# Performance work log

Measured on AMD Instinct MI355X. Metric: run time of the kernel, lower is better.

The kernel has to match this reference:

```python
import jax, jax.numpy as jnp
import numpy as np

DIM, N_HEADS, N_KV, HEAD_DIM = 4096, 32, 8, 128
REPEATS = N_HEADS // N_KV
SCALE = HEAD_DIM ** -0.5


def apply_rope(x, offset=0):
    # x: [b, h, l, hd]; rotation convention matches the torch source:
    # out_even = xe*cos + xo*sin, out_odd = -xe*sin + xo*cos, interleaved back.
    hd = x.shape[-1]
    l = x.shape[2]
    freqs = 1.0 / 10000.0 ** (jnp.arange(0, hd, 2, dtype=jnp.float32) / hd)  # [hd/2]
    t = jnp.arange(l, dtype=jnp.float32) + offset
    ang = t[:, None] * freqs[None, :]                     # [l, hd/2]
    sin, cos = jnp.sin(ang), jnp.cos(ang)
    xe, xo = x[..., 0::2], x[..., 1::2]                   # [b,h,l,hd/2]
    out = jnp.stack([xe * cos + xo * sin, -xe * sin + xo * cos], axis=-1)
    return out.reshape(x.shape)


def setup_inputs() -> dict:
    key = jax.random.key(0)
    ks = jax.random.split(key, 5)
    b, l = 1, 2048
    x = jax.random.normal(ks[0], (b, l, DIM), dtype=jnp.float32)
    # additive causal mask: 0 on/below diagonal, -1e9 above
    neg = jnp.full((l, l), -1e9, dtype=jnp.float32)
    mask = jnp.triu(neg, k=1)
    wq = jax.random.normal(ks[1], (N_HEADS * HEAD_DIM, DIM), dtype=jnp.float32) * 0.02
    wk = jax.random.normal(ks[2], (N_KV * HEAD_DIM, DIM), dtype=jnp.float32) * 0.02
    wv = jax.random.normal(ks[3], (N_KV * HEAD_DIM, DIM), dtype=jnp.float32) * 0.02
    wo = jax.random.normal(ks[4], (DIM, N_HEADS * HEAD_DIM), dtype=jnp.float32) * 0.02
    return {"x": x, "mask": mask, "wq": wq, "wk": wk, "wv": wv, "wo": wo}


def reference(x, mask, wq, wk, wv, wo):
    b, l, d = x.shape
    q = (x @ wq.T).reshape(b, l, N_HEADS, HEAD_DIM).transpose(0, 2, 1, 3)  # [b,H,l,hd]
    k = (x @ wk.T).reshape(b, l, N_KV, HEAD_DIM).transpose(0, 2, 1, 3)     # [b,Hk,l,hd]
    v = (x @ wv.T).reshape(b, l, N_KV, HEAD_DIM).transpose(0, 2, 1, 3)
    # GQA repeat (head = kv_head*repeats + r, same as torch cat+view)
    k = jnp.repeat(k, REPEATS, axis=1)
    v = jnp.repeat(v, REPEATS, axis=1)
    q = apply_rope(q)
    k = apply_rope(k)
    atn = jnp.einsum('bhqd,bhkd->bhqk', q * SCALE, k) + mask
    atn = jax.nn.softmax(atn.astype(jnp.float32), axis=-1).astype(q.dtype)
    out = jnp.einsum('bhqk,bhkd->bhqd', atn, v)
    out = out.transpose(0, 2, 1, 3).reshape(b, l, -1)
    return (out @ wo.T, k, v)
```

## Files before the change

kernel.cpp:

```cpp
#include <hip/hip_runtime.h>
#include <stdint.h>

#define L_SEQ  2048
#define NHEAD  32
#define NKV    8
#define HD     128
#define DIM    4096
#define KVDIM  1024
#define QKVS   6144
#define SCALE  0.08838834764831845f
#define LOG2E  1.4426950408889634f
#define SM_OFF 12.0f

typedef __attribute__((ext_vector_type(8))) short bf16x8;
typedef __attribute__((ext_vector_type(4))) float f32x4;

__device__ __forceinline__ unsigned short f2bf(float f) {
    unsigned u = __float_as_uint(f);
    u = (u + 0x7FFFu + ((u >> 16) & 1u)) >> 16;
    return (unsigned short)u;
}
__device__ __forceinline__ float bf2f(unsigned short h) {
    return __uint_as_float(((unsigned)h) << 16);
}
__device__ __forceinline__ void gload_lds16(const void* g, void* l) {
    __builtin_amdgcn_global_load_lds(
        (const __attribute__((address_space(1))) unsigned int*)g,
        (__attribute__((address_space(3))) unsigned int*)l, 16, 0, 0);
}

__global__ void cvt_f32_bf16(const float* __restrict__ in, unsigned short* __restrict__ out, int n4) {
    int i = blockIdx.x * blockDim.x + threadIdx.x;
    int stride = gridDim.x * blockDim.x;
    for (; i < n4; i += stride) {
        float4 v = ((const float4*)in)[i];
        ushort4 o;
        o.x = f2bf(v.x); o.y = f2bf(v.y); o.z = f2bf(v.z); o.w = f2bf(v.w);
        ((ushort4*)out)[i] = o;
    }
}

__global__ void addf32(float* __restrict__ out, const float* __restrict__ p, int n4) {
    int i = blockIdx.x * blockDim.x + threadIdx.x;
    int stride = gridDim.x * blockDim.x;
    for (; i < n4; i += stride) {
        float4 a = ((const float4*)out)[i];
        float4 b = ((const float4*)p)[i];
        a.x += b.x; a.y += b.y; a.z += b.z; a.w += b.w;
        ((float4*)out)[i] = a;
    }
}

__global__ void rope_table(float2* __restrict__ rt) {
    int i = blockIdx.x * blockDim.x + threadIdx.x;
    if (i >= L_SEQ * 64) return;
    int l = i >> 6, f = i & 63;
    float freq = powf(10000.0f, -(float)f / 64.0f);
    float ang  = (float)l * freq;
    rt[i] = make_float2(cosf(ang), sinf(ang));
}

__global__ void rope_apply(unsigned short* __restrict__ X, const float2* __restrict__ rt,
                           int log2H, int strideShorts, float mul) {
    int i = blockIdx.x * blockDim.x + threadIdx.x;
    int f  = i & 63;
    int hh = (i >> 6) & ((1 << log2H) - 1);
    int l  = i >> (6 + log2H);
    if (l >= L_SEQ) return;
    float2 cs = rt[(l << 6) + f];
    size_t base = (size_t)l * strideShorts + (hh << 7);
    float xe = bf2f(X[base + 2 * f]);
    float xo = bf2f(X[base + 2 * f + 1]);
    X[base + 2 * f]     = f2bf((xe * cs.x + xo * cs.y) * mul);
    X[base + 2 * f + 1] = f2bf((-xe * cs.y + xo * cs.x) * mul);
}

__global__ void kv_out(const unsigned short* __restrict__ KVp,
                       float* __restrict__ KO, float* __restrict__ VO) {
    int i = blockIdx.x * blockDim.x + threadIdx.x;
    if (i >= L_SEQ * KVDIM) return;
    int d  = i & 127;
    int h8 = (i >> 7) & 7;
    int l  = i >> 10;
    float kv = bf2f(KVp[(size_t)l * QKVS + h8 * HD + d]);
    float vv = bf2f(KVp[(size_t)l * QKVS + KVDIM + h8 * HD + d]);
#pragma unroll
    for (int r = 0; r < 4; ++r) {
        int h = h8 * 4 + r;
        KO[((size_t)h * L_SEQ + l) * HD + d] = kv;
        VO[((size_t)h * L_SEQ + l) * HD + d] = vv;
    }
}

__global__ void vtrans(const unsigned short* __restrict__ KVp, unsigned short* __restrict__ VT) {
    __shared__ unsigned short t[32][33];
    int lt = blockIdx.x * 32;
    int h8 = blockIdx.y >> 2;
    int dt = (blockIdx.y & 3) * 32;
    int tx = threadIdx.x & 31, ty = threadIdx.x >> 5;
#pragma unroll
    for (int yy = ty; yy < 32; yy += 8)
        t[yy][tx] = KVp[(size_t)(lt + yy) * QKVS + KVDIM + h8 * HD + dt + tx];
    __syncthreads();
#pragma unroll
    for (int yy = ty; yy < 32; yy += 8)
        VT[(size_t)(h8 * HD + dt + yy) * L_SEQ + lt + tx] = t[tx][yy];
}

template <typename OT>
__global__ __launch_bounds__(512, 2) void gemm_8ph(const unsigned short* __restrict__ A,
                                                   const unsigned short* __restrict__ B,
                                                   OT* __restrict__ C0, OT* __restrict__ C1,
                                                   int N, int K, int klen) {
    __shared__ __align__(16) char L[131072];
    const int tid = threadIdx.x;
    const int w = tid >> 6, lane = tid & 63;
    const int gx = gridDim.x;
    const int nwg = gx * gridDim.y;
    const int orig = blockIdx.y * gx + blockIdx.x;
    const int swz = (orig & 7) * (nwg >> 3) + (orig >> 3);
    const int m0 = (swz / gx) * 256, n0 = (swz % gx) * 256;
    const int kbase = blockIdx.z * klen;
    OT* __restrict__ C = blockIdx.z ? C1 : C0;
    const int wr = (w >> 2) & 1;
    const int wc = w & 3;
    const int lr = lane & 15, lg = lane >> 4;
    const int NKT = klen >> 6;

    auto stageA = [&](int slot, int half, int kt) {
#pragma unroll
        for (int c = 0; c < 2; ++c) {
            int rl = half * 128 + w * 16 + c * 8;
            int r  = rl + (lane >> 3);
            int cg = (lane & 7) ^ (r & 7);
            gload_lds16(A + (size_t)(m0 + r) * K + kbase + kt * 64 + cg * 8,
                        L + slot * 32768 + rl * 128);
        }
    };
    auto stageB = [&](int slot, int half, int kt) {
#pragma unroll
        for (int c = 0; c < 2; ++c) {
            int rl = half * 128 + w * 16 + c * 8;
            int r  = rl + (lane >> 3);
            int cg = (lane & 7) ^ (r & 7);
            gload_lds16(B + (size_t)(n0 + r) * K + kbase + kt * 64 + cg * 8,
                        L + 65536 + slot * 32768 + rl * 128);
        }
    };

    const f32x4 fz = {0.f, 0.f, 0.f, 0.f};
    f32x4 acc[8][4];
#pragma unroll
    for (int m = 0; m < 8; ++m)
#pragma unroll
        for (int n = 0; n < 4; ++n) acc[m][n] = fz;

    stageA(0, 0, 0); stageA(0, 1, 0); stageB(0, 0, 0); stageB(0, 1, 0);
    if (NKT > 1) { stageB(1, 0, 1); stageB(1, 1, 1); }
    asm volatile("s_waitcnt vmcnt(4)" ::: "memory");
    __builtin_amdgcn_s_barrier();

    const int swb = (lr & 7) << 4;
    bf16x8 bfrag[4][2];
    for (int kt = 0; kt < NKT; ++kt) {
        const int s = kt & 1;
        const char* Abase = L + s * 32768;
        const char* Bbase = L + 65536 + s * 32768;
#pragma unroll
        for (int q = 0; q < 4; ++q) {
            bf16x8 af[2][2];
#pragma unroll
            for (int mm = 0; mm < 2; ++mm)
#pragma unroll
                for (int kk = 0; kk < 2; ++kk) {
                    int r = wr * 128 + (q * 2 + mm) * 16 + lr;
                    int b = (kk * 64 + lg * 16) ^ swb;
                    af[mm][kk] = *(const bf16x8*)(Abase + r * 128 + b);
                }
            if (q == 0) {
#pragma unroll
                for (int n = 0; n < 4; ++n)
#pragma unroll
                    for (int kk = 0; kk < 2; ++kk) {
                        int r = wc * 64 + n * 16 + lr;
                        int b = (kk * 64 + lg * 16) ^ swb;
                        bfrag[n][kk] = *(const bf16x8*)(Bbase + r * 128 + b);
                    }
            }
            if (q == 0 && kt + 1 < NKT) stageA(s ^ 1, 0, kt + 1);
            if (q == 1 && kt + 1 < NKT) stageA(s ^ 1, 1, kt + 1);
            if (q == 2 && kt + 2 < NKT) stageB(s, 0, kt + 2);
            if (q == 3) {
                if (kt + 2 < NKT) stageB(s, 1, kt + 2);
                asm volatile("s_waitcnt vmcnt(4)" ::: "memory");
            }
            __builtin_amdgcn_s_barrier();
            asm volatile("s_waitcnt lgkmcnt(0)" ::: "memory");
            __builtin_amdgcn_sched_barrier(0);
            __builtin_amdgcn_s_setprio(1);
#pragma unroll
            for (int mm = 0; mm < 2; ++mm)
#pragma unroll
                for (int n = 0; n < 4; ++n)
#pragma unroll
                    for (int kk = 0; kk < 2; ++kk)
                        acc[q * 2 + mm][n] = __builtin_amdgcn_mfma_f32_16x16x32_bf16(
                            af[mm][kk], bfrag[n][kk], acc[q * 2 + mm][n], 0, 0, 0);
            __builtin_amdgcn_s_setprio(0);
            __builtin_amdgcn_s_barrier();
        }
    }
#pragma unroll
    for (int m = 0; m < 8; ++m) {
        int mrow = m0 + wr * 128 + m * 16 + lg * 4;
#pragma unroll
        for (int n = 0; n < 4; ++n) {
            int ncol = n0 + wc * 64 + n * 16 + lr;
#pragma unroll
            for (int r = 0; r < 4; ++r) {
                float v = acc[m][n][r];
                if constexpr (sizeof(OT) == 2) C[(size_t)(mrow + r) * N + ncol] = f2bf(v);
                else                           C[(size_t)(mrow + r) * N + ncol] = v;
            }
        }
    }
}

__global__ __launch_bounds__(128) void attn_fwd(const unsigned short* __restrict__ Q,
                                                const unsigned short* __restrict__ KVp,
                                                const unsigned short* __restrict__ VT,
                                                unsigned short* __restrict__ AO) {
    __shared__ __align__(16) unsigned short Ks[64 * 128];
    __shared__ __align__(16) unsigned short Vs[128 * 64];
    __shared__ __align__(16) unsigned short P[2][2][16][64];
    const int tid = threadIdx.x, w = tid >> 6, lane = tid & 63;
    const int idx = blockIdx.x;
    const int h8  = idx & 7;
    const int h   = (h8 << 2) + ((idx >> 3) & 3);
    const int u   = idx >> 5;
    const int t   = u & 7, quart = u >> 3;
    const int qb  = (quart == 0) ? 31 - t : (quart == 1) ? 16 + t
                  : (quart == 2) ? 15 - t : t;
    const int lr = lane & 15, lg = lane >> 4;
    const int r0 = qb * 64 + w * 32;

    bf16x8 qf[2][4];
#pragma unroll
    for (int f = 0; f < 2; ++f) {
        const unsigned short* qrow = Q + (size_t)(r0 + f * 16 + lr) * QKVS + h * HD + lg * 8;
#pragma unroll
        for (int kd = 0; kd < 4; ++kd) qf[f][kd] = *(const bf16x8*)(qrow + kd * 32);
    }

    bf16x8 ones;
#pragma unroll
    for (int z = 0; z < 8; ++z) ones[z] = (short)0x3F80;

    const f32x4 fz = {0.f, 0.f, 0.f, 0.f};
    f32x4 o[2][9];
#pragma unroll
    for (int f = 0; f < 2; ++f)
#pragma unroll
        for (int nd = 0; nd < 9; ++nd) o[f][nd] = fz;

    const int nkv = qb + 1;
    for (int kv = 0; kv < nkv; ++kv) {
        const int kv0 = kv * 64;
#pragma unroll
        for (int c = 0; c < 8; ++c) {
            int krow = w * 32 + c * 4 + (lane >> 4);
            int kcg  = (lane & 15) ^ (krow & 7);
            gload_lds16(KVp + (size_t)(kv0 + krow) * QKVS + h8 * HD + kcg * 8,
                        Ks + (w * 32 + c * 4) * 128);
            int vrow = w * 64 + c * 8 + (lane >> 3);
            int vcg  = (lane & 7) ^ (vrow & 7);
            gload_lds16(VT + (size_t)(h8 * HD + vrow) * L_SEQ + kv0 + vcg * 8,
                        Vs + (w * 64 + c * 8) * 64);
        }
        __syncthreads();
        f32x4 s[2][4];
#pragma unroll
        for (int f = 0; f < 2; ++f)
#pragma unroll
            for (int ni = 0; ni < 4; ++ni) s[f][ni] = fz;
        __builtin_amdgcn_s_setprio(1);
#pragma unroll
        for (int ni = 0; ni < 4; ++ni) {
            bf16x8 kf[4];
#pragma unroll
            for (int kd = 0; kd < 4; ++kd)
                kf[kd] = *(const bf16x8*)(Ks + (ni * 16 + lr) * 128 +
                                          (((kd * 4 + lg) ^ (lr & 7)) * 8));
#pragma unroll
            for (int f = 0; f < 2; ++f)
#pragma unroll
                for (int kd = 0; kd < 4; ++kd)
                    s[f][ni] = __builtin_amdgcn_mfma_f32_16x16x32_bf16(qf[f][kd], kf[kd], s[f][ni], 0, 0, 0);
        }
        __builtin_amdgcn_s_setprio(0);
#pragma unroll
        for (int f = 0; f < 2; ++f) {
            const int rbase = r0 + f * 16;
            const bool need_mask = (kv0 + 63) > rbase;
#pragma unroll
            for (int ni = 0; ni < 4; ++ni)
#pragma unroll
                for (int rr = 0; rr < 4; ++rr) {
                    float p = __builtin_amdgcn_exp2f(s[f][ni][rr] - SM_OFF);
                    if (need_mask) {
                        int col = kv0 + ni * 16 + lr;
                        int row = rbase + lg * 4 + rr;
                        p = (col > row) ? 0.f : p;
                    }
                    s[f][ni][rr] = p;
                }
            char* Pb = (char*)&P[w][f][0][0];
#pragma unroll
            for (int ni = 0; ni < 4; ni += 2)
#pragma unroll
                for (int rr = 0; rr < 4; ++rr) {
                    unsigned pk;
                    asm("v_cvt_pk_bf16_f32 %0, %1, %2" : "=v"(pk) : "v"(s[f][ni][rr]), "v"(s[f][ni + 1][rr]));
                    const int row = lg * 4 + rr;
                    const int sw = (row & 7) << 4;
                    *(unsigned short*)(Pb + ((row * 128 + (ni * 16 + lr) * 2) ^ sw)) = (unsigned short)pk;
                    *(unsigned short*)(Pb + ((row * 128 + ((ni + 1) * 16 + lr) * 2) ^ sw)) =
                        (unsigned short)(pk >> 16);
                }
        }
        bf16x8 pa[2][2];
        const int swr = (lr & 7) << 4;
#pragma unroll
        for (int f = 0; f < 2; ++f) {
            const char* Pb = (const char*)&P[w][f][0][0];
#pragma unroll
            for (int ks = 0; ks < 2; ++ks)
                pa[f][ks] = *(const bf16x8*)(Pb + ((lr * 128 + ks * 64 + lg * 16) ^ swr));
        }
        __builtin_amdgcn_s_setprio(1);
#pragma unroll
        for (int nd = 0; nd < 8; ++nd) {
            bf16x8 vf[2];
#pragma unroll
            for (int ks = 0; ks < 2; ++ks)
                vf[ks] = *(const bf16x8*)(Vs + (nd * 16 + lr) * 64 +
                                          (((ks * 4 + lg) ^ (lr & 7)) * 8));
#pragma unroll
            for (int f = 0; f < 2; ++f)
#pragma unroll
                for (int ks = 0; ks < 2; ++ks)
                    o[f][nd] = __builtin_amdgcn_mfma_f32_16x16x32_bf16(pa[f][ks], vf[ks], o[f][nd], 0, 0, 0);
        }
#pragma unroll
        for (int f = 0; f < 2; ++f)
#pragma unroll
            for (int ks = 0; ks < 2; ++ks)
                o[f][8] = __builtin_amdgcn_mfma_f32_16x16x32_bf16(pa[f][ks], ones, o[f][8], 0, 0, 0);
        __builtin_amdgcn_s_setprio(0);
        __syncthreads();
    }
#pragma unroll
    for (int f = 0; f < 2; ++f) {
        float inv[4];
#pragma unroll
        for (int rr = 0; rr < 4; ++rr) inv[rr] = 1.0f / o[f][8][rr];
#pragma unroll
        for (int nd = 0; nd < 8; ++nd)
#pragma unroll
            for (int rr = 0; rr < 4; ++rr) {
                int row = r0 + f * 16 + lg * 4 + rr;
                AO[(size_t)row * DIM + h * HD + nd * 16 + lr] = f2bf(o[f][nd][rr] * inv[rr]);
            }
    }
}

extern "C" void kernel_launch(void* const* d_in, const int* in_sizes, int n_in,
                              void* d_out, int out_size, void* d_ws, size_t ws_size,
                              hipStream_t stream) {
    (void)in_sizes; (void)n_in; (void)out_size; (void)ws_size;
    const float* x  = (const float*)d_in[0];
    const float* wq = (const float*)d_in[2];
    const float* wk = (const float*)d_in[3];
    const float* wv = (const float*)d_in[4];
    const float* wo = (const float*)d_in[5];

    float* out = (float*)d_out;
    float* KO  = out + (size_t)L_SEQ * DIM;
    float* VO  = KO + (size_t)NHEAD * L_SEQ * HD;

    char* ws = (char*)d_ws;
    const size_t MB = 1024 * 1024;
    unsigned short* xb   = (unsigned short*)(ws);
    unsigned short* wqb  = (unsigned short*)(ws + 16 * MB);
    unsigned short* wkvb = (unsigned short*)(ws + 48 * MB);
    unsigned short* qkvp = (unsigned short*)(ws + 64 * MB);
    unsigned short* vtb  = (unsigned short*)(ws + 88 * MB);
    float2*         rt   = (float2*)(ws + 92 * MB);
    unsigned short* aob  = xb;
    unsigned short* wob  = wqb;
    unsigned short* kvp  = qkvp + KVDIM * 4;
    float*          pko  = (float*)(ws + 48 * MB);

    cvt_f32_bf16<<<2048, 256, 0, stream>>>(x,  xb,  L_SEQ * DIM / 4);
    cvt_f32_bf16<<<2048, 256, 0, stream>>>(wq, wqb, DIM * DIM / 4);
    cvt_f32_bf16<<<2048, 256, 0, stream>>>(wk, wkvb, KVDIM * DIM / 4);
    cvt_f32_bf16<<<2048, 256, 0, stream>>>(wv, wkvb + (size_t)KVDIM * DIM, KVDIM * DIM / 4);
    rope_table<<<(L_SEQ * 64) / 256, 256, 0, stream>>>(rt);

    gemm_8ph<unsigned short><<<dim3(QKVS / 256, L_SEQ / 256, 1), 512, 0, stream>>>(
        xb, wqb, qkvp, qkvp, QKVS, DIM, DIM);
    cvt_f32_bf16<<<2048, 256, 0, stream>>>(wo, wob, DIM * DIM / 4);

    rope_apply<<<(L_SEQ * NHEAD * 64) / 256, 256, 0, stream>>>(qkvp, rt, 5, QKVS, SCALE * LOG2E);
    rope_apply<<<(L_SEQ * NKV * 64) / 256, 256, 0, stream>>>(kvp, rt, 3, QKVS, 1.0f);

    kv_out<<<(L_SEQ * KVDIM) / 256, 256, 0, stream>>>(kvp, KO, VO);
    vtrans<<<dim3(L_SEQ / 32, 32), 256, 0, stream>>>(kvp, vtb);

    attn_fwd<<<1024, 128, 0, stream>>>(qkvp, kvp, vtb, aob);

    gemm_8ph<float><<<dim3(DIM / 256, L_SEQ / 256, 2), 512, 0, stream>>>(
        aob, wob, out, pko, DIM, DIM, DIM / 2);
    addf32<<<2048, 256, 0, stream>>>(out, pko, L_SEQ * DIM / 4);
}
```

Before: 345.9 us.

## Double-buffer A fragments in registers to overlap LDS reads with MFMA

Restructures the GEMM main loop so the A-fragment LDS reads for the next quarter, and for the next k-tile's first quarter, are issued before the MFMA block of the current quarter. It also unrolls k-tiles in pairs so the LDS slot index is a compile-time constant. The global-to-LDS staging points and vmcnt waits are reordered to fit the new schedule. The aim is to hide LDS read latency behind matrix math. It costs extra VGPRs for the second fragment buffer, and the removed explicit lgkmcnt waits and sched_barriers leave ordering to the compiler, which risks correctness or spills under launch_bounds(512,2). The paired loop also assumes NKT is even.

```diff
diff --git a/kernel.cpp b/kernel.cpp
--- a/kernel.cpp
+++ b/kernel.cpp
@@ -126,6 +126,7 @@
     const int wc = w & 3;
     const int lr = lane & 15, lg = lane >> 4;
     const int NKT = klen >> 6;
+    const int swb = (lr & 7) << 4;
 
     auto stageA = [&](int slot, int half, int kt) {
 #pragma unroll
@@ -155,58 +156,81 @@
 #pragma unroll
         for (int n = 0; n < 4; ++n) acc[m][n] = fz;
 
+    bf16x8 af0[2][2], af1[2][2];
+    bf16x8 bfr[4][2];
+
+    auto readA = [&](bf16x8 (&dst)[2][2], const char* base, int q) {
+#pragma unroll
+        for (int mm = 0; mm < 2; ++mm)
+#pragma unroll
+            for (int kk = 0; kk < 2; ++kk) {
+                int r = wr * 128 + (q * 2 + mm) * 16 + lr;
+                int b = (kk * 64 + lg * 16) ^ swb;
+                dst[mm][kk] = *(const bf16x8*)(base + r * 128 + b);
+            }
+    };
+    auto readB = [&](const char* base) {
+#pragma unroll
+        for (int n = 0; n < 4; ++n)
+#pragma unroll
+            for (int kk = 0; kk < 2; ++kk) {
+                int r = wc * 64 + n * 16 + lr;
+                int b = (kk * 64 + lg * 16) ^ swb;
+                bfr[n][kk] = *(const bf16x8*)(base + r * 128 + b);
+            }
+    };
+    auto mfma16 = [&](int q, bf16x8 (&a)[2][2]) {
+        __builtin_amdgcn_s_setprio(1);
+#pragma unroll
+        for (int mm = 0; mm < 2; ++mm)
+#pragma unroll
+            for (int n = 0; n < 4; ++n)
+#pragma unroll
+                for (int kk = 0; kk < 2; ++kk)
+                    acc[q * 2 + mm][n] = __builtin_amdgcn_mfma_f32_16x16x32_bf16(
+                        a[mm][kk], bfr[n][kk], acc[q * 2 + mm][n], 0, 0, 0);
+        __builtin_amdgcn_s_setprio(0);
+    };
+
     stageA(0, 0, 0); stageA(0, 1, 0); stageB(0, 0, 0); stageB(0, 1, 0);
     if (NKT > 1) { stageB(1, 0, 1); stageB(1, 1, 1); }
     asm volatile("s_waitcnt vmcnt(4)" ::: "memory");
     __builtin_amdgcn_s_barrier();
-
-    const int swb = (lr & 7) << 4;
-    bf16x8 bfrag[4][2];
-    for (int kt = 0; kt < NKT; ++kt) {
-        const int s = kt & 1;
-        const char* Abase = L + s * 32768;
-        const char* Bbase = L + 65536 + s * 32768;
-#pragma unroll
-        for (int q = 0; q < 4; ++q) {
-            bf16x8 af[2][2];
-#pragma unroll
-            for (int mm = 0; mm < 2; ++mm)
-#pragma unroll
-                for (int kk = 0; kk < 2; ++kk) {
-                    int r = wr * 128 + (q * 2 + mm) * 16 + lr;
-                    int b = (kk * 64 + lg * 16) ^ swb;
-                    af[mm][kk] = *(const bf16x8*)(Abase + r * 128 + b);
-                }
-            if (q == 0) {
-#pragma unroll
-                for (int n = 0; n < 4; ++n)
-#pragma unroll
-                    for (int kk = 0; kk < 2; ++kk) {
-                        int r = wc * 64 + n * 16 + lr;
-                        int b = (kk * 64 + lg * 16) ^ swb;
-                        bfrag[n][kk] = *(const bf16x8*)(Bbase + r * 128 + b);
-                    }
+    readA(af0, L + 0, 0);
+
+    for (int kt0 = 0; kt0 < NKT; kt0 += 2) {
+#pragma unroll
+        for (int kp = 0; kp < 2; ++kp) {
+            const int kt = kt0 + kp;
+            const int s = kp;
+            const char* Abase = L + s * 32768;
+            const char* Bbase = L + 65536 + s * 32768;
+            const char* AbaseN = L + (s ^ 1) * 32768;
+            readB(Bbase);
+            readA(af1, Abase, 1);
+            if (kt + 1 < NKT) stageA(s ^ 1, 0, kt + 1);
+            __builtin_amdgcn_s_barrier();
+            mfma16(0, af0);
+            __builtin_amdgcn_s_barrier();
+            readA(af0, Abase, 2);
+            if (kt + 1 < NKT) stageA(s ^ 1, 1, kt + 1);
+            __builtin_amdgcn_s_barrier();
+            mfma16(1, af1);
+            __builtin_amdgcn_s_barrier();
+            readA(af1, Abase, 3);
+            if (kt + 2 < NKT) {
+                stageB(s, 0, kt + 2);
+                asm volatile("s_waitcnt vmcnt(2)" ::: "memory");
+            } else {
+                asm volatile("s_waitcnt vmcnt(0)" ::: "memory");
             }
-            if (q == 0 && kt + 1 < NKT) stageA(s ^ 1, 0, kt + 1);
-            if (q == 1 && kt + 1 < NKT) stageA(s ^ 1, 1, kt + 1);
-            if (q == 2 && kt + 2 < NKT) stageB(s, 0, kt + 2);
-            if (q == 3) {
-                if (kt + 2 < NKT) stageB(s, 1, kt + 2);
-                asm volatile("s_waitcnt vmcnt(4)" ::: "memory");
-            }
-            __builtin_amdgcn_s_barrier();
-            asm volatile("s_waitcnt lgkmcnt(0)" ::: "memory");
-            __builtin_amdgcn_sched_barrier(0);
-            __builtin_amdgcn_s_setprio(1);
-#pragma unroll
-            for (int mm = 0; mm < 2; ++mm)
-#pragma unroll
-                for (int n = 0; n < 4; ++n)
-#pragma unroll
-                    for (int kk = 0; kk < 2; ++kk)
-                        acc[q * 2 + mm][n] = __builtin_amdgcn_mfma_f32_16x16x32_bf16(
-                            af[mm][kk], bfrag[n][kk], acc[q * 2 + mm][n], 0, 0, 0);
-            __builtin_amdgcn_s_setprio(0);
+            __builtin_amdgcn_s_barrier();
+            mfma16(2, af0);
+            __builtin_amdgcn_s_barrier();
+            if (kt + 1 < NKT) readA(af0, AbaseN, 0);
+            if (kt + 2 < NKT) stageB(s, 1, kt + 2);
+            __builtin_amdgcn_s_barrier();
+            mfma16(3, af1);
             __builtin_amdgcn_s_barrier();
         }
     }
```

Measured after the change: 350.5 us. Within noise of the previous version (+1.3%).
